# Optimization experiments

Measured on AMD Instinct MI355X. Metric: run time of the kernel, lower is better.

## Reference

```python
import jax, jax.numpy as jnp
import numpy as np

D_ATTN = 64

def setup_inputs() -> dict:
    key = jax.random.key(0)
    k1, k2, k3 = jax.random.split(key, 3)
    B, N, d_ffn = 8, 2048, 1536
    x = jax.random.normal(k1, (B, N, d_ffn), dtype=jnp.float32)
    W_qkv = jax.random.normal(k2, (d_ffn, 3 * D_ATTN), dtype=jnp.float32) * (1.0 / np.sqrt(d_ffn))
    b_qkv = jnp.zeros((3 * D_ATTN,), dtype=jnp.float32)
    W_out = jax.random.normal(k3, (D_ATTN, d_ffn // 2), dtype=jnp.float32) * (1.0 / np.sqrt(D_ATTN))
    b_out = jnp.zeros((d_ffn // 2,), dtype=jnp.float32)
    return {"x": x, "W_qkv": W_qkv, "b_qkv": b_qkv, "W_out": W_out, "b_out": b_out}

def reference(x, W_qkv, b_qkv, W_out, b_out):
    # x: [B, N, d_ffn]
    qkv = jnp.einsum('bnd,de->bne', x, W_qkv) + b_qkv  # [B, N, 3*d_attn]
    q, k, v = jnp.split(qkv, 3, axis=-1)               # each [B, N, d_attn]
    scale = 1.0 / jnp.sqrt(jnp.float32(D_ATTN))
    energy = jnp.einsum('bqd,bkd->bqk', q, k) * scale  # [B, N, N]
    attn = jax.nn.softmax(energy, axis=-1)
    out = jnp.einsum('bqk,bkd->bqd', attn, v)          # [B, N, d_attn]
    out = jnp.einsum('bnd,de->bne', out, W_out) + b_out  # [B, N, d_ffn//2]
    return out
```

## Files before the change

kernel.cpp:

```cpp
#include <hip/hip_runtime.h>
#include <hip/hip_bf16.h>


typedef __attribute__((ext_vector_type(8))) short short8;
typedef __attribute__((ext_vector_type(4))) short short4v;
typedef __attribute__((ext_vector_type(4))) float float4v;
typedef __attribute__((ext_vector_type(16))) float float16v;

#define MFMA16(a, b, c) __builtin_amdgcn_mfma_f32_16x16x32_bf16((a), (b), (c), 0, 0, 0)
#define MFMA32(a, b, c) __builtin_amdgcn_mfma_f32_32x32x16_bf16((a), (b), (c), 0, 0, 0)

#define LDS_BARRIER() asm volatile("s_waitcnt lgkmcnt(0)\n\ts_barrier" ::: "memory")

static __device__ __forceinline__ void plswap(unsigned& a, unsigned& b) {
  asm("v_permlane32_swap_b32 %0, %1" : "+v"(a), "+v"(b));
}

static __device__ __forceinline__ unsigned short f2bf(float x) {
  union { float f; unsigned u; } v; v.f = x;
  return (unsigned short)((v.u + 0x7FFFu + ((v.u >> 16) & 1u)) >> 16);
}
static __device__ __forceinline__ short8 ldg8(const short* p) {
  return *(const short8*)p;
}

__global__ __launch_bounds__(256) void k_prep(
    const float* __restrict__ Wq, const float* __restrict__ Wo,
    short* __restrict__ Wtf, short* __restrict__ WtO) {
  __shared__ float wl[64 * 52];
  __shared__ __align__(16) short tl[64 * 72];
  const int tid = threadIdx.x;
  int id = blockIdx.x;
  if (id < 96) {
    const int kk = id >> 2, w = id & 3;
    const int r = tid >> 2, cq = (tid & 3) * 12;
    const float* sp = Wq + (size_t)(kk * 64 + r) * 192 + w * 48 + cq;
    float4v a = *(const float4v*)(sp);
    float4v b = *(const float4v*)(sp + 4);
    float4v c4 = *(const float4v*)(sp + 8);
    float* dp = wl + r * 52 + cq;
    *(float4v*)(dp) = a; *(float4v*)(dp + 4) = b; *(float4v*)(dp + 8) = c4;
    __syncthreads();
#pragma unroll
    for (int i = 0; i < 2; ++i) {
      const int fid = i * 256 + tid;
      if (fid < 384) {
        const int frag = fid >> 6, lane = fid & 63;
        const int lo = lane & 15, hi = lane >> 4;
        const int c = frag >> 1, ks = frag & 1;
        short8 o;
#pragma unroll
        for (int e = 0; e < 8; ++e)
          o[e] = (short)f2bf(wl[(ks * 32 + hi * 8 + e) * 52 + c * 16 + lo]);
        *(short8*)(Wtf + ((((size_t)kk * 4 + w) * 6 + frag) << 9) + lane * 8) = o;
      }
    }
  } else {
    id -= 96;
    const int r = tid >> 2, cq = (tid & 3) * 16;
    const float* sp = Wo + (size_t)r * 768 + id * 64 + cq;
    float4v v0 = *(const float4v*)(sp);
    float4v v1 = *(const float4v*)(sp + 4);
    float4v v2 = *(const float4v*)(sp + 8);
    float4v v3 = *(const float4v*)(sp + 12);
    short8 s0, s1;
#pragma unroll
    for (int i = 0; i < 4; ++i) {
      s0[i] = (short)f2bf(v0[i]); s0[i + 4] = (short)f2bf(v1[i]);
      s1[i] = (short)f2bf(v2[i]); s1[i + 4] = (short)f2bf(v3[i]);
    }
    *(short8*)(tl + r * 72 + cq) = s0;
    *(short8*)(tl + r * 72 + cq + 8) = s1;
    __syncthreads();
    short8 o0, o1;
#pragma unroll
    for (int j = 0; j < 8; ++j) {
      o0[j] = tl[(cq + j) * 72 + r];
      o1[j] = tl[(cq + 8 + j) * 72 + r];
    }
    short* dp2 = WtO + (size_t)(id * 64 + r) * 64 + cq;
    *(short8*)(dp2) = o0;
    *(short8*)(dp2 + 8) = o1;
  }
}

__global__ __launch_bounds__(256) void k_qkv(
    const float* __restrict__ x, const short* __restrict__ Wtf,
    const float* __restrict__ bq, short* __restrict__ Qf,
    short* __restrict__ Kf, short* __restrict__ Vf) {
  __shared__ __align__(16) short xl[4][32 * 72];
  const int tid = threadIdx.x;
  const int w = tid >> 6, lane = tid & 63, lo = lane & 15, hi = lane >> 4;
  const int m0 = blockIdx.x * 32;
  const float KSC = 0.18033688011112042f;
  const int cb = w * 48;

  float4v acc[2][3];
#pragma unroll
  for (int r = 0; r < 2; ++r)
#pragma unroll
    for (int c = 0; c < 3; ++c) acc[r][c] = (float4v)0.0f;

  const int xr = tid >> 3, xc = (tid & 7) * 8;
  const float* xrow = x + (size_t)(m0 + xr) * 1536 + xc;
  const int xlo = xr * 72 + xc;
  const short* wbase = Wtf + ((size_t)w * 6) * 512 + lane * 8;

  short8 wA[6], wB[6];
  float4v xs0[2], xs1[2], xs2[2], xs3[2];

#define ISSUE_X(KK, S)                                                         \
  do { S[0] = *(const float4v*)(xrow + (KK) * 64);                             \
       S[1] = *(const float4v*)(xrow + (KK) * 64 + 4); } while (0)
#define ISSUE_W(KK, WS)                                                        \
  do { const short* _wp = wbase + (size_t)(KK) * 12288;                        \
       _Pragma("unroll")                                                       \
       for (int _f = 0; _f < 6; ++_f) WS[_f] = ldg8(_wp + _f * 512); } while (0)
#define WRITE_X(S, B)                                                          \
  do { short8 _sv;                                                             \
       _Pragma("unroll")                                                       \
       for (int _j = 0; _j < 4; ++_j) {                                        \
         _sv[_j] = (short)f2bf(S[0][_j]);                                      \
         _sv[_j + 4] = (short)f2bf(S[1][_j]);                                  \
       }                                                                       \
       *(short8*)(&xl[B][xlo]) = _sv; } while (0)
#define COMPUTE(B, WS)                                                         \
  do { const short* _xb = &xl[B][0];                                           \
       _Pragma("unroll")                                                       \
       for (int _r = 0; _r < 2; ++_r) {                                        \
         short8 _a0 = *(const short8*)(_xb + (_r * 16 + lo) * 72 + hi * 8);    \
         short8 _a1 = *(const short8*)(_xb + (_r * 16 + lo) * 72 + 32 + hi * 8);\
         _Pragma("unroll")                                                     \
         for (int _c = 0; _c < 3; ++_c) {                                      \
           acc[_r][_c] = MFMA16(_a0, WS[2 * _c], acc[_r][_c]);                 \
           acc[_r][_c] = MFMA16(_a1, WS[2 * _c + 1], acc[_r][_c]);             \
         }                                                                     \
       } } while (0)

  ISSUE_X(0, xs0);
  ISSUE_X(1, xs1);
  ISSUE_X(2, xs2);
  ISSUE_W(0, wA);
  ISSUE_W(1, wB);
  WRITE_X(xs0, 0);
  LDS_BARRIER();

  for (int k4 = 0; k4 < 24; k4 += 4) {
    COMPUTE(0, wA);
    ISSUE_W(k4 + 2, wA);
    if (k4 + 3 < 24) ISSUE_X(k4 + 3, xs3);
    WRITE_X(xs1, 1);
    LDS_BARRIER();
    COMPUTE(1, wB);
    ISSUE_W(k4 + 3, wB);
    if (k4 + 4 < 24) ISSUE_X(k4 + 4, xs0);
    WRITE_X(xs2, 2);
    LDS_BARRIER();
    COMPUTE(2, wA);
    if (k4 + 4 < 24) ISSUE_W(k4 + 4, wA);
    if (k4 + 5 < 24) ISSUE_X(k4 + 5, xs1);
    if (k4 + 3 < 24) WRITE_X(xs3, 3);
    LDS_BARRIER();
    COMPUTE(3, wB);
    if (k4 + 5 < 24) ISSUE_W(k4 + 5, wB);
    if (k4 + 6 < 24) ISSUE_X(k4 + 6, xs2);
    if (k4 + 4 < 24) WRITE_X(xs0, 0);
    LDS_BARRIER();
  }
#undef ISSUE_X
#undef ISSUE_W
#undef WRITE_X
#undef COMPUTE

  float bb[3];
#pragma unroll
  for (int c = 0; c < 3; ++c) bb[c] = bq[cb + c * 16 + lo];

  const int b = m0 >> 11;
  const int row0 = m0 & 2047;
  short* qbuf = &xl[0][0];
  short* kstg = &xl[1][0];
  short* vstg = &xl[2][0];

#pragma unroll
  for (int r = 0; r < 2; ++r)
#pragma unroll
    for (int c = 0; c < 3; ++c) {
      const int colb = cb + c * 16;
      short* buf = (colb < 64) ? qbuf : ((colb < 128) ? kstg : vstg);
      const int d0 = (colb & 63) + lo;
#pragma unroll
      for (int j = 0; j < 4; ++j) {
        float vv = acc[r][c][j] + bb[c];
        if (colb < 64) vv *= KSC;
        buf[(r * 16 + hi * 4 + j) * 72 + d0] = (short)f2bf(vv);
      }
    }
  LDS_BARRIER();

  {
    const int rr = tid >> 3, dq = (tid & 7) * 8;
    const int t32 = row0 >> 5, i = dq >> 4, h = (dq >> 3) & 1;
    const size_t base = ((((size_t)b * 64 + t32) * 4 + i) * 2 + h) * 256 + rr * 8;
    *(short8*)(Qf + base) = *(const short8*)(qbuf + rr * 72 + dq);
    *(short8*)(Kf + base) = *(const short8*)(kstg + rr * 72 + dq);
  }

  {
    const int dr = tid >> 2, kq8 = (tid & 3) * 8;
    short8 o0;
#pragma unroll
    for (int j = 0; j < 8; ++j) o0[j] = vstg[(kq8 + j) * 72 + dr];
    const int kg = row0 >> 5, s = (kq8 >> 4) & 1, h = (kq8 >> 3) & 1;
    const int dc = dr >> 5, c32 = dr & 31;
    short* vp = Vf + ((((((size_t)b * 64 + kg) * 2 + dc) * 2 + s) * 2 + h) * 32 + c32) * 8;
    *(short8*)(vp) = o0;
  }
}

__global__ __launch_bounds__(512) void k_attn(
    const short* __restrict__ Qf, const short* __restrict__ Kf,
    const short* __restrict__ Vf, short* __restrict__ att) {
  __shared__ float Od[8][32][76];
  __shared__ float Ol[8][32];
  const int tid = threadIdx.x;
  const int w = tid >> 6, lane = tid & 63;
  const int c = lane & 31, h = lane >> 5;
  const int b = blockIdx.x >> 6;
  const int qg = blockIdx.x & 63;
  const size_t g0 = (size_t)b * 2048 + qg * 32;

  short8 qf0 = ldg8(Qf + (((size_t)b * 64 + qg) * 4 + 0) * 512 + lane * 8);
  short8 qf1 = ldg8(Qf + (((size_t)b * 64 + qg) * 4 + 1) * 512 + lane * 8);
  short8 qf2 = ldg8(Qf + (((size_t)b * 64 + qg) * 4 + 2) * 512 + lane * 8);
  short8 qf3 = ldg8(Qf + (((size_t)b * 64 + qg) * 4 + 3) * 512 + lane * 8);

  float lp = 0.0f;
  float16v acc0 = (float16v)0.0f;
  float16v acc1 = (float16v)0.0f;

  int kg = w * 8;
  const short* kb = Kf + ((size_t)b * 64) * 2048 + lane * 8;
  const short* vb = Vf + ((size_t)b * 64) * 2048 + lane * 8;

#define ATTN_STEP(K0, K1, K2, K3, V0, V1, V2, V3)                              \
  do {                                                                         \
    float16v sf = (float16v)0.0f;                                              \
    sf = MFMA32(K0, qf0, sf);                                                  \
    sf = MFMA32(K1, qf1, sf);                                                  \
    sf = MFMA32(K2, qf2, sf);                                                  \
    sf = MFMA32(K3, qf3, sf);                                                  \
    unsigned wpk[8];                                                           \
    _Pragma("unroll")                                                          \
    for (int m = 0; m < 8; ++m) {                                              \
      float p0 = __builtin_amdgcn_exp2f(sf[2 * m]);                            \
      float p1 = __builtin_amdgcn_exp2f(sf[2 * m + 1]);                        \
      unsigned u0 = __builtin_bit_cast(unsigned, p0) & 0xFFFF0000u;            \
      unsigned u1 = __builtin_bit_cast(unsigned, p1) & 0xFFFF0000u;            \
      lp += __builtin_bit_cast(float, u0) + __builtin_bit_cast(float, u1);     \
      wpk[m] = (u0 >> 16) | u1;                                                \
    }                                                                          \
    plswap(wpk[0], wpk[2]);                                                    \
    plswap(wpk[1], wpk[3]);                                                    \
    plswap(wpk[4], wpk[6]);                                                    \
    plswap(wpk[5], wpk[7]);                                                    \
    union { unsigned u[4]; short8 s8; } bt0, bt1;                              \
    bt0.u[0] = wpk[0]; bt0.u[1] = wpk[1]; bt0.u[2] = wpk[2]; bt0.u[3] = wpk[3];\
    bt1.u[0] = wpk[4]; bt1.u[1] = wpk[5]; bt1.u[2] = wpk[6]; bt1.u[3] = wpk[7];\
    acc0 = MFMA32(V0, bt0.s8, acc0);                                           \
    acc0 = MFMA32(V1, bt1.s8, acc0);                                           \
    acc1 = MFMA32(V2, bt0.s8, acc1);                                           \
    acc1 = MFMA32(V3, bt1.s8, acc1);                                           \
  } while (0)

  const short* kpA = kb + (size_t)kg * 2048;
  const short* vpA = vb + (size_t)kg * 2048;
  short8 ka0 = ldg8(kpA), ka1 = ldg8(kpA + 512), ka2 = ldg8(kpA + 1024), ka3 = ldg8(kpA + 1536);
  short8 va0 = ldg8(vpA), va1 = ldg8(vpA + 512), va2 = ldg8(vpA + 1024), va3 = ldg8(vpA + 1536);

  for (int t = 0; t < 8; t += 2) {
    const short* kpB = kb + (size_t)(kg + 1) * 2048;
    const short* vpB = vb + (size_t)(kg + 1) * 2048;
    short8 kb0 = ldg8(kpB), kb1 = ldg8(kpB + 512), kb2 = ldg8(kpB + 1024), kb3 = ldg8(kpB + 1536);
    short8 vb0 = ldg8(vpB), vb1 = ldg8(vpB + 512), vb2 = ldg8(vpB + 1024), vb3 = ldg8(vpB + 1536);

    ATTN_STEP(ka0, ka1, ka2, ka3, va0, va1, va2, va3);

    if (t + 2 < 8) {
      const short* kpN = kb + (size_t)(kg + 2) * 2048;
      const short* vpN = vb + (size_t)(kg + 2) * 2048;
      ka0 = ldg8(kpN); ka1 = ldg8(kpN + 512); ka2 = ldg8(kpN + 1024); ka3 = ldg8(kpN + 1536);
      va0 = ldg8(vpN); va1 = ldg8(vpN + 512); va2 = ldg8(vpN + 1024); va3 = ldg8(vpN + 1536);
    }

    ATTN_STEP(kb0, kb1, kb2, kb3, vb0, vb1, vb2, vb3);
    kg += 2;
  }
#undef ATTN_STEP

  lp += __shfl_xor(lp, 32, 64);

#pragma unroll
  for (int g = 0; g < 4; ++g) {
    float4v a0, a1;
#pragma unroll
    for (int r = 0; r < 4; ++r) { a0[r] = acc0[4 * g + r]; a1[r] = acc1[4 * g + r]; }
    *(float4v*)(&Od[w][c][8 * g + 4 * h]) = a0;
    *(float4v*)(&Od[w][c][32 + 8 * g + 4 * h]) = a1;
  }
  if (h == 0) Ol[w][c] = lp;
  __syncthreads();

  {
    const int q = tid >> 4, dq = (tid & 15) * 4;
    float L = 0.0f;
    float4v o = (float4v)0.0f;
#pragma unroll
    for (int w2 = 0; w2 < 8; ++w2) {
      L += Ol[w2][q];
      o += *(const float4v*)(&Od[w2][q][dq]);
    }
    const float inv = 1.0f / L;
    short4v r;
#pragma unroll
    for (int j = 0; j < 4; ++j) r[j] = (short)f2bf(o[j] * inv);
    *(short4v*)(att + (g0 + q) * 64 + dq) = r;
  }
}

__global__ __launch_bounds__(256) void k_out(
    const short* __restrict__ att, const short* __restrict__ WtO,
    const float* __restrict__ bo, float* __restrict__ out) {
  const int tid = threadIdx.x;
  const int w = tid >> 6, lane = tid & 63, lo = lane & 15, hi = lane >> 4;
  const int wc = w * 192;
  const int m0 = blockIdx.x * 32;

  short8 af[2][2];
#pragma unroll
  for (int rf = 0; rf < 2; ++rf) {
    const short* ap = att + (size_t)(m0 + rf * 16 + lo) * 64 + hi * 8;
    af[rf][0] = ldg8(ap);
    af[rf][1] = ldg8(ap + 32);
  }
  float4v acc[2][12];
#pragma unroll
  for (int rf = 0; rf < 2; ++rf)
#pragma unroll
    for (int c = 0; c < 12; ++c) acc[rf][c] = (float4v)0.0f;

#pragma unroll
  for (int c = 0; c < 12; ++c) {
    const short* bp = WtO + (size_t)(wc + c * 16 + lo) * 64 + hi * 8;
    short8 b0 = ldg8(bp);
    short8 b1 = ldg8(bp + 32);
#pragma unroll
    for (int rf = 0; rf < 2; ++rf) {
      acc[rf][c] = MFMA16(af[rf][0], b0, acc[rf][c]);
      acc[rf][c] = MFMA16(af[rf][1], b1, acc[rf][c]);
    }
  }
#pragma unroll
  for (int c = 0; c < 12; ++c) {
    const float bb = bo[wc + c * 16 + lo];
#pragma unroll
    for (int rf = 0; rf < 2; ++rf)
#pragma unroll
      for (int j = 0; j < 4; ++j)
        out[(size_t)(m0 + rf * 16 + hi * 4 + j) * 768 + wc + c * 16 + lo] =
            acc[rf][c][j] + bb;
  }
}

extern "C" void kernel_launch(void* const* d_in, const int* in_sizes, int n_in,
                              void* d_out, int out_size, void* d_ws, size_t ws_size,
                              hipStream_t stream) {
  (void)in_sizes; (void)n_in; (void)out_size; (void)ws_size;
  const float* x  = (const float*)d_in[0];
  const float* Wq = (const float*)d_in[1];
  const float* bq = (const float*)d_in[2];
  const float* Wo = (const float*)d_in[3];
  const float* bo = (const float*)d_in[4];
  float* out = (float*)d_out;

  char* ws = (char*)d_ws;
  short* Qf  = (short*)(ws);
  short* Kf  = (short*)(ws + 2097152);
  short* Vf  = (short*)(ws + 4194304);
  short* att = (short*)(ws + 6291456);
  short* Wtf = (short*)(ws + 8388608);
  short* WtO = (short*)(ws + 8978432);

  k_prep<<<108, 256, 0, stream>>>(Wq, Wo, Wtf, WtO);
  k_qkv<<<512, 256, 0, stream>>>(x, Wtf, bq, Qf, Kf, Vf);
  k_attn<<<512, 512, 0, stream>>>(Qf, Kf, Vf, att);
  k_out<<<512, 256, 0, stream>>>(att, WtO, bo, out);
}
```

Baseline: 62.95 us.

## Stream x tiles into LDS with direct global-to-LDS DMA and XOR swizzle

```diff
diff --git a/kernel.cpp b/kernel.cpp
--- a/kernel.cpp
+++ b/kernel.cpp
@@ -11,6 +11,14 @@
 #define MFMA32(a, b, c) __builtin_amdgcn_mfma_f32_32x32x16_bf16((a), (b), (c), 0, 0, 0)
 
 #define LDS_BARRIER() asm volatile("s_waitcnt lgkmcnt(0)\n\ts_barrier" ::: "memory")
+#define BAR_VM16() asm volatile("s_waitcnt vmcnt(16) lgkmcnt(0)\n\ts_barrier" ::: "memory")
+#define BAR_VM0()  asm volatile("s_waitcnt vmcnt(0) lgkmcnt(0)\n\ts_barrier" ::: "memory")
+
+static __device__ __forceinline__ void gload_lds16(const float* g, float* l) {
+  __builtin_amdgcn_global_load_lds(
+      (const __attribute__((address_space(1))) void*)g,
+      (__attribute__((address_space(3))) void*)l, 16, 0, 0);
+}
 
 static __device__ __forceinline__ void plswap(unsigned& a, unsigned& b) {
   asm("v_permlane32_swap_b32 %0, %1" : "+v"(a), "+v"(b));
@@ -19,6 +27,12 @@
 static __device__ __forceinline__ unsigned short f2bf(float x) {
   union { float f; unsigned u; } v; v.f = x;
   return (unsigned short)((v.u + 0x7FFFu + ((v.u >> 16) & 1u)) >> 16);
+}
+static __device__ __forceinline__ short8 cvt8(float4v a, float4v b) {
+  short8 s;
+#pragma unroll
+  for (int j = 0; j < 4; ++j) { s[j] = (short)f2bf(a[j]); s[j + 4] = (short)f2bf(b[j]); }
+  return s;
 }
 static __device__ __forceinline__ short8 ldg8(const short* p) {
   return *(const short8*)p;
@@ -88,7 +102,7 @@
     const float* __restrict__ x, const short* __restrict__ Wtf,
     const float* __restrict__ bq, short* __restrict__ Qf,
     short* __restrict__ Kf, short* __restrict__ Vf) {
-  __shared__ __align__(16) short xl[4][32 * 72];
+  __shared__ __align__(16) float xf[4][32 * 64];
   const int tid = threadIdx.x;
   const int w = tid >> 6, lane = tid & 63, lo = lane & 15, hi = lane >> 4;
   const int m0 = blockIdx.x * 32;
@@ -101,75 +115,62 @@
 #pragma unroll
     for (int c = 0; c < 3; ++c) acc[r][c] = (float4v)0.0f;
 
-  const int xr = tid >> 3, xc = (tid & 7) * 8;
-  const float* xrow = x + (size_t)(m0 + xr) * 1536 + xc;
-  const int xlo = xr * 72 + xc;
   const short* wbase = Wtf + ((size_t)w * 6) * 512 + lane * 8;
-
   short8 wA[6], wB[6];
-  float4v xs0[2], xs1[2], xs2[2], xs3[2];
-
-#define ISSUE_X(KK, S)                                                         \
-  do { S[0] = *(const float4v*)(xrow + (KK) * 64);                             \
-       S[1] = *(const float4v*)(xrow + (KK) * 64 + 4); } while (0)
+
+#define DMA(KK, B)                                                             \
+  do {                                                                         \
+    _Pragma("unroll")                                                          \
+    for (int _j = 0; _j < 2; ++_j) {                                           \
+      const int _r = 8 * w + 4 * _j + (lane >> 4);                             \
+      const int _g = (lane & 15) ^ (_r & 15);                                  \
+      gload_lds16(x + (size_t)(m0 + _r) * 1536 + (KK) * 64 + _g * 4,           \
+                  &xf[B][(8 * w + 4 * _j) * 64]);                              \
+    }                                                                          \
+  } while (0)
+
 #define ISSUE_W(KK, WS)                                                        \
   do { const short* _wp = wbase + (size_t)(KK) * 12288;                        \
        _Pragma("unroll")                                                       \
        for (int _f = 0; _f < 6; ++_f) WS[_f] = ldg8(_wp + _f * 512); } while (0)
-#define WRITE_X(S, B)                                                          \
-  do { short8 _sv;                                                             \
-       _Pragma("unroll")                                                       \
-       for (int _j = 0; _j < 4; ++_j) {                                        \
-         _sv[_j] = (short)f2bf(S[0][_j]);                                      \
-         _sv[_j + 4] = (short)f2bf(S[1][_j]);                                  \
-       }                                                                       \
-       *(short8*)(&xl[B][xlo]) = _sv; } while (0)
+
 #define COMPUTE(B, WS)                                                         \
-  do { const short* _xb = &xl[B][0];                                           \
-       _Pragma("unroll")                                                       \
-       for (int _r = 0; _r < 2; ++_r) {                                        \
-         short8 _a0 = *(const short8*)(_xb + (_r * 16 + lo) * 72 + hi * 8);    \
-         short8 _a1 = *(const short8*)(_xb + (_r * 16 + lo) * 72 + 32 + hi * 8);\
-         _Pragma("unroll")                                                     \
-         for (int _c = 0; _c < 3; ++_c) {                                      \
-           acc[_r][_c] = MFMA16(_a0, WS[2 * _c], acc[_r][_c]);                 \
-           acc[_r][_c] = MFMA16(_a1, WS[2 * _c + 1], acc[_r][_c]);             \
-         }                                                                     \
-       } } while (0)
-
-  ISSUE_X(0, xs0);
-  ISSUE_X(1, xs1);
-  ISSUE_X(2, xs2);
+  do { const float* _xb = &xf[B][0];                                           \
+    _Pragma("unroll")                                                          \
+    for (int _r = 0; _r < 2; ++_r) {                                           \
+      const float* _rp = _xb + (_r * 16 + lo) * 64;                            \
+      float4v _g0 = *(const float4v*)(_rp + ((2 * hi) ^ lo) * 4);              \
+      float4v _g1 = *(const float4v*)(_rp + ((2 * hi + 1) ^ lo) * 4);          \
+      float4v _g2 = *(const float4v*)(_rp + ((8 + 2 * hi) ^ lo) * 4);          \
+      float4v _g3 = *(const float4v*)(_rp + ((8 + 2 * hi + 1) ^ lo) * 4);      \
+      short8 _a0 = cvt8(_g0, _g1);                                             \
+      short8 _a1 = cvt8(_g2, _g3);                                             \
+      _Pragma("unroll")                                                        \
+      for (int _c = 0; _c < 3; ++_c) {                                         \
+        acc[_r][_c] = MFMA16(_a0, WS[2 * _c], acc[_r][_c]);                    \
+        acc[_r][_c] = MFMA16(_a1, WS[2 * _c + 1], acc[_r][_c]);                \
+      }                                                                        \
+    } } while (0)
+
+  DMA(0, 0);
+  DMA(1, 1);
+  DMA(2, 2);
   ISSUE_W(0, wA);
   ISSUE_W(1, wB);
-  WRITE_X(xs0, 0);
-  LDS_BARRIER();
-
-  for (int k4 = 0; k4 < 24; k4 += 4) {
-    COMPUTE(0, wA);
-    ISSUE_W(k4 + 2, wA);
-    if (k4 + 3 < 24) ISSUE_X(k4 + 3, xs3);
-    WRITE_X(xs1, 1);
-    LDS_BARRIER();
-    COMPUTE(1, wB);
-    ISSUE_W(k4 + 3, wB);
-    if (k4 + 4 < 24) ISSUE_X(k4 + 4, xs0);
-    WRITE_X(xs2, 2);
-    LDS_BARRIER();
-    COMPUTE(2, wA);
-    if (k4 + 4 < 24) ISSUE_W(k4 + 4, wA);
-    if (k4 + 5 < 24) ISSUE_X(k4 + 5, xs1);
-    if (k4 + 3 < 24) WRITE_X(xs3, 3);
-    LDS_BARRIER();
-    COMPUTE(3, wB);
-    if (k4 + 5 < 24) ISSUE_W(k4 + 5, wB);
-    if (k4 + 6 < 24) ISSUE_X(k4 + 6, xs2);
-    if (k4 + 4 < 24) WRITE_X(xs0, 0);
-    LDS_BARRIER();
-  }
-#undef ISSUE_X
+  BAR_VM0();
+
+  for (int k4 = 0; k4 < 20; k4 += 4) {
+    COMPUTE(0, wA); ISSUE_W(k4 + 2, wA); DMA(k4 + 3, 3); BAR_VM16();
+    COMPUTE(1, wB); ISSUE_W(k4 + 3, wB); DMA(k4 + 4, 0); BAR_VM16();
+    COMPUTE(2, wA); ISSUE_W(k4 + 4, wA); DMA(k4 + 5, 1); BAR_VM16();
+    COMPUTE(3, wB); ISSUE_W(k4 + 5, wB); DMA(k4 + 6, 2); BAR_VM16();
+  }
+  COMPUTE(0, wA); ISSUE_W(22, wA); DMA(23, 3); BAR_VM0();
+  COMPUTE(1, wB); ISSUE_W(23, wB); BAR_VM0();
+  COMPUTE(2, wA); BAR_VM0();
+  COMPUTE(3, wB); BAR_VM0();
+#undef DMA
 #undef ISSUE_W
-#undef WRITE_X
 #undef COMPUTE
 
   float bb[3];
@@ -178,9 +179,10 @@
 
   const int b = m0 >> 11;
   const int row0 = m0 & 2047;
-  short* qbuf = &xl[0][0];
-  short* kstg = &xl[1][0];
-  short* vstg = &xl[2][0];
+  short* sbase = (short*)&xf[0][0];
+  short* qbuf = sbase;
+  short* kstg = sbase + 2304;
+  short* vstg = sbase + 4608;
 
 #pragma unroll
   for (int r = 0; r < 2; ++r)
```

Result: slower. 66.70 us (+5.9%).
